# Optimization experiments

Measured on AMD Instinct MI355X. Metric: run time of the kernel, lower is better.

## Reference

```python
import jax, jax.numpy as jnp
import numpy as np
from jax import lax

# --- block geometry (matches init_kwargs) ---
B = 8
DIM = 192
HEADS = 6
KEY_DIM = DIM // HEADS  # 32, attn_ratio=1 so d == key_dim and dh == DIM
HX, WX = 32, 32         # search region
HZ, WZ = 16, 16         # template region
T = 1                   # template_number
L = HX * WX + T * HZ * WZ  # 1280 tokens
MLP_HIDDEN = int(DIM * 4.0)
BN_EPS = 1e-5


def _build_bias_idx():
    """Replicates Attention.__init__ global_att=True bias-index construction.
    Unique-offset ids may be permuted vs torch dict-insertion order, which is an
    equivalent reparameterization of the (randomly initialized) bias table."""
    g = np.stack(np.meshgrid(np.arange(HX), np.arange(WX), indexing='ij'), -1).reshape(-1, 2)
    pts = [g]
    for i in range(T):
        r = np.arange(HX + HZ * i, WX + WZ * (i + 1))
        g2 = np.stack(np.meshgrid(r, r, indexing='ij'), -1).reshape(-1, 2)
        pts.append(g2)
    p = np.concatenate(pts, 0)                      # (L, 2)
    off = np.abs(p[:, None, :] - p[None, :, :])     # (L, L, 2)
    key = off[:, :, 0].astype(np.int64) * 4096 + off[:, :, 1]
    uniq, inv = np.unique(key, return_inverse=True)
    return inv.reshape(L, L).astype(np.int32), int(len(uniq))


def setup_inputs() -> dict:
    key = jax.random.key(0)
    ks = jax.random.split(key, 16)
    idx_np, n_off = _build_bias_idx()
    s = 0.02
    return {
        'xz': jax.random.normal(ks[0], (B, L, DIM), jnp.float32),
        'bias_idx': jnp.asarray(idx_np),
        'ln1_g': jnp.ones((DIM,), jnp.float32),
        'ln1_b': jnp.zeros((DIM,), jnp.float32),
        'wqkv': jax.random.normal(ks[1], (DIM, 3 * DIM), jnp.float32) * s,
        'bqkv': jnp.zeros((3 * DIM,), jnp.float32),
        'wproj': jax.random.normal(ks[2], (DIM, DIM), jnp.float32) * s,
        'bproj': jnp.zeros((DIM,), jnp.float32),
        'bias_table': jax.random.normal(ks[3], (HEADS, n_off), jnp.float32) * 0.1,
        'conv_w': jax.random.normal(ks[4], (3, 3, 1, DIM), jnp.float32) * 0.1,  # depthwise HWIO
        'bn_scale': jnp.ones((DIM,), jnp.float32) + jax.random.normal(ks[5], (DIM,), jnp.float32) * 0.01,
        'bn_bias': jax.random.normal(ks[6], (DIM,), jnp.float32) * 0.01,
        'ln2_g': jnp.ones((DIM,), jnp.float32),
        'ln2_b': jnp.zeros((DIM,), jnp.float32),
        'w1': jax.random.normal(ks[7], (DIM, MLP_HIDDEN), jnp.float32) * s,
        'b1': jnp.zeros((MLP_HIDDEN,), jnp.float32),
        'w2': jax.random.normal(ks[8], (MLP_HIDDEN, DIM), jnp.float32) * s,
        'b2': jnp.zeros((DIM,), jnp.float32),
    }


def _layernorm(x, g, b, eps=1e-5):
    mu = jnp.mean(x, -1, keepdims=True)
    var = jnp.mean(jnp.square(x - mu), -1, keepdims=True)
    return (x - mu) * lax.rsqrt(var + eps) * g + b


def reference(xz, bias_idx, ln1_g, ln1_b, wqkv, bqkv, wproj, bproj, bias_table,
              conv_w, bn_scale, bn_bias, ln2_g, ln2_b, w1, b1, w2, b2):
    Bn, N, D = xz.shape
    scale = KEY_DIM ** -0.5
    # --- Attention (LeViT-style with gathered relative-position bias) ---
    h = _layernorm(xz, ln1_g, ln1_b)
    qkv = (h @ wqkv + bqkv).reshape(Bn, N, HEADS, 3 * KEY_DIM)
    q, k, v = jnp.split(qkv, 3, axis=3)            # each (B, N, H, key_dim)
    bias = bias_table[:, bias_idx]                  # (H, N, N) gather
    attn = jnp.einsum('bnhd,bmhd->bhnm', q, k) * scale + bias
    attn = jax.nn.softmax(attn, axis=-1)
    o = jnp.einsum('bhnm,bmhd->bnhd', attn, v).reshape(Bn, N, D)
    xm = xz + o @ wproj + bproj
    # --- depthwise local conv (Conv2d_BN, BN folded to scale/bias) per segment ---
    segs = []
    start = 0
    for (Hh, Ww) in [(HX, WX)] + [(HZ, WZ)] * T:
        xc = xm[:, start:start + Hh * Ww, :].reshape(Bn, Hh, Ww, D)
        xc = lax.conv_general_dilated(
            xc, conv_w, window_strides=(1, 1), padding='SAME',
            dimension_numbers=('NHWC', 'HWIO', 'NHWC'), feature_group_count=D)
        xc = xc * bn_scale + bn_bias
        segs.append(xc.reshape(Bn, Hh * Ww, D))
        start += Hh * Ww
    xm = jnp.concatenate(segs, axis=1)
    # --- MLP with pre-LN (exact GELU, matching nn.GELU default) ---
    m = _layernorm(xm, ln2_g, ln2_b)
    m = jax.nn.gelu(m @ w1 + b1, approximate=False) @ w2 + b2
    return xm + m
```

## Files before the change

### kernel.cpp

```cpp
#include <hip/hip_runtime.h>
#include <hip/hip_bf16.h>

#define BATCH 8
#define LTOK 1280
#define DIMC 192
#define HEADS 6
#define KD 32
#define HID 768
#define NROWS (BATCH*LTOK)

typedef short s16x8 __attribute__((ext_vector_type(8)));
typedef float f32x4 __attribute__((ext_vector_type(4)));
typedef unsigned short u16;

#define QS (0.17677669529663687f * 1.4426950408889634f)
#define L2E 1.4426950408889634f

__device__ __forceinline__ u16 f2bf(float x) {
    unsigned u = __float_as_uint(x);
    u = (u + 0x7FFFu + ((u >> 16) & 1u)) >> 16;
    return (u16)u;
}
__device__ __forceinline__ float bflo(unsigned u) { return __uint_as_float(u << 16); }
__device__ __forceinline__ float bfhi(unsigned u) { return __uint_as_float(u & 0xffff0000u); }
__device__ __forceinline__ float fexp2(float x) { float r; asm("v_exp_f32 %0, %1" : "=v"(r) : "v"(x)); return r; }
__device__ __forceinline__ float frcp(float x)  { float r; asm("v_rcp_f32 %0, %1" : "=v"(r) : "v"(x)); return r; }

__global__ __launch_bounds__(256) void pre_kernel(const float* w0, const float* w1,
                                                  const float* w2, const float* w3,
                                                  u16* o0, u16* o1, u16* o2, u16* o3,
                                                  const int* __restrict__ bidx,
                                                  const float* __restrict__ btab,
                                                  int n_off, u16* __restrict__ bm,
                                                  const float* __restrict__ xz,
                                                  const float* __restrict__ ln1g,
                                                  const float* __restrict__ ln1b,
                                                  u16* __restrict__ hbuf) {
    __shared__ float s[16][17];
    int f = blockIdx.x;
    if (f >= 3328) {
        int row = (f - 3328) * 4 + (threadIdx.x >> 6);
        int lane = threadIdx.x & 63;
        const float* xr = xz + (size_t)row * DIMC;
        float v0 = xr[lane], v1 = xr[lane + 64], v2 = xr[lane + 128];
        float sm = v0 + v1 + v2;
        float ss = v0 * v0 + v1 * v1 + v2 * v2;
        #pragma unroll
        for (int off = 32; off; off >>= 1) {
            sm += __shfl_xor(sm, off);
            ss += __shfl_xor(ss, off);
        }
        float mu  = sm * (1.0f / DIMC);
        float var = ss * (1.0f / DIMC) - mu * mu;
        float inv = rsqrtf(var + 1e-5f);
        u16* yr = hbuf + (size_t)row * DIMC;
        yr[lane]       = f2bf((v0 - mu) * inv * ln1g[lane]       + ln1b[lane]);
        yr[lane + 64]  = f2bf((v1 - mu) * inv * ln1g[lane + 64]  + ln1b[lane + 64]);
        yr[lane + 128] = f2bf((v2 - mu) * inv * ln1g[lane + 128] + ln1b[lane + 128]);
        return;
    }
    if (f >= 1728) {
        size_t flat = (size_t)(f - 1728) * 1024 + (size_t)threadIdx.x * 4;
        int4 iv = *(const int4*)(bidx + flat);
        #pragma unroll
        for (int h = 0; h < HEADS; ++h) {
            const float* tab = btab + (size_t)h * n_off;
            ushort4 o;
            o.x = f2bf(tab[iv.x] * L2E);
            o.y = f2bf(tab[iv.y] * L2E);
            o.z = f2bf(tab[iv.z] * L2E);
            o.w = f2bf(tab[iv.w] * L2E);
            *(ushort4*)(bm + (size_t)h * (LTOK * LTOK) + flat) = o;
        }
        return;
    }
    const float* in; u16* out; int K, N, tn, tk;
    if (f < 432)       { in = w0; out = o0; K = 192; N = 576; int r = f;        tn = r % 36; tk = r / 36; }
    else if (f < 576)  { in = w1; out = o1; K = 192; N = 192; int r = f - 432;  tn = r % 12; tk = r / 12; }
    else if (f < 1152) { in = w2; out = o2; K = 192; N = 768; int r = f - 576;  tn = r % 48; tk = r / 48; }
    else               { in = w3; out = o3; K = 768; N = 192; int r = f - 1152; tn = r % 12; tk = r / 12; }
    int tx = threadIdx.x & 15, ty = threadIdx.x >> 4;
    s[ty][tx] = in[(size_t)(tk * 16 + ty) * N + tn * 16 + tx];
    __syncthreads();
    out[(size_t)(tn * 16 + ty) * K + tk * 16 + tx] = f2bf(s[tx][ty]);
}

template<int ACT, int RES, int OBF, int QKV, int K, int MTILE>
__global__ __launch_bounds__(256) void gemm_mfma(const u16* __restrict__ A,
                                                 const u16* __restrict__ Wt,
                                                 const float* __restrict__ bias,
                                                 const float* __restrict__ R,
                                                 void* __restrict__ Cp,
                                                 u16* __restrict__ qb,
                                                 u16* __restrict__ kp,
                                                 u16* __restrict__ vp,
                                                 int N) {
    constexpr int SUB = MTILE / 64;
    int tid = threadIdx.x;
    int L = tid & 63, w = tid >> 6;
    int r = L & 15, g = L >> 4;
    int m0 = blockIdx.y * MTILE + w * (16 * SUB);
    int n0 = blockIdx.x * 64;

    f32x4 acc[SUB][4] = {};
    const u16* Ab = A + (size_t)(m0 + r) * K + g * 8;
    const u16* Wb = Wt + (size_t)(n0 + r) * K + g * 8;
    #pragma unroll 6
    for (int k0 = 0; k0 < K; k0 += 32) {
        s16x8 af[SUB];
        #pragma unroll
        for (int mi = 0; mi < SUB; ++mi)
            af[mi] = *(const s16x8*)(Ab + (size_t)mi * 16 * K + k0);
        #pragma unroll
        for (int nn = 0; nn < 4; ++nn) {
            s16x8 bf = *(const s16x8*)(Wb + (size_t)nn * 16 * K + k0);
            #pragma unroll
            for (int mi = 0; mi < SUB; ++mi)
                acc[mi][nn] = __builtin_amdgcn_mfma_f32_16x16x32_bf16(af[mi], bf, acc[mi][nn], 0, 0, 0);
        }
    }

    #pragma unroll
    for (int mi = 0; mi < SUB; ++mi)
    #pragma unroll
    for (int nn = 0; nn < 4; ++nn) {
        int cb = n0 + nn * 16;
        #pragma unroll
        for (int i = 0; i < 4; ++i) {
            int row = m0 + mi * 16 + g * 4 + i;
            float v = acc[mi][nn][i] + bias[cb + r];
            if (QKV) {
                int h  = cb / 96, c0 = cb % 96;
                int reg = c0 >> 5;
                if (reg == 0) {
                    v *= QS;
                    qb[(size_t)row * DIMC + h * 32 + (c0 & 31) + r] = f2bf(v);
                } else {
                    int b_ = row / LTOK, t = row - b_ * LTOK;
                    int T = t >> 5, it = t & 31;
                    int d = (c0 & 31) + r;
                    if (reg == 1) {
                        int which = (it >> 2) & 1;
                        int ik = ((it >> 3) << 2) | (it & 3);
                        int Lk = ((d >> 3) << 4) + ik;
                        kp[((size_t)(b_ * HEADS + h) * 40 + T) * 1024 + which * 512 + Lk * 8 + (d & 7)] = f2bf(v);
                    } else {
                        int Lv = ((it >> 3) << 4) + (d & 15);
                        vp[((size_t)(b_ * HEADS + h) * 40 + T) * 1024 + (d >> 4) * 512 + Lv * 8 + (it & 7)] = f2bf(v);
                    }
                }
            } else {
                if (ACT == 1) {
                    float u = v;
                    float y = 0.7978845608028654f * (u + 0.044715f * u * u * u);
                    float e2 = fexp2(y * 2.885390081777927f);
                    v = u - u * frcp(e2 + 1.0f);
                }
                if (RES) v += R[(size_t)row * N + cb + r];
                if (OBF) ((u16*)Cp)[(size_t)row * N + cb + r] = f2bf(v);
                else     ((float*)Cp)[(size_t)row * N + cb + r] = v;
            }
        }
    }
}

__global__ __launch_bounds__(256) void attn_mfma(const u16* __restrict__ qb,
                                                 const u16* __restrict__ kp,
                                                 const u16* __restrict__ vp,
                                                 const u16* __restrict__ bm,
                                                 u16* __restrict__ ob) {
    __shared__ __align__(16) u16 kvs[2][2][2048];
    int tid = threadIdx.x;
    int L = tid & 63, w = tid >> 6;
    int r = L & 15, g = L >> 4;
    int L8 = L * 8;

    int bid = blockIdx.x;
    int work = (bid & 7) * 120 + (bid >> 3);
    int b  = work & 7;
    int hq = work >> 3;
    int qt = (hq % 20) * 4 + w;
    int h  = hq / 20;

    s16x8 qf = *(const s16x8*)(qb + (size_t)(b * LTOK + qt * 16 + r) * DIMC + h * 32 + g * 8);

    int skv = w >> 1, half = w & 1;
    const u16* gs = (skv ? vp : kp) + (size_t)(b * HEADS + h) * 40 * 1024 + L8;
    u16* dst0 = &kvs[0][skv][half * 1024 + L8];
    u16* dst1 = &kvs[1][skv][half * 1024 + L8];

    const u16* bmr = bm + ((size_t)h * LTOK + qt * 16 + r) * LTOK + g * 8;

    f32x4 acc0 = {0.f, 0.f, 0.f, 0.f}, acc1 = {0.f, 0.f, 0.f, 0.f};
    float lsum = 0.f;

    {
        int4 pA = *(const int4*)(gs + half * 1024);
        int4 pB = *(const int4*)(gs + half * 1024 + 512);
        *(int4*)dst0 = pA;
        *(int4*)(dst0 + 512) = pB;
    }
    int4 bv0 = *(const int4*)(bmr);
    int4 bv1 = *(const int4*)(bmr + 32);
    __syncthreads();

    #pragma unroll 1
    for (int T = 0; T < 20; ++T) {
        int4 nA, nB, nb0, nb1;
        if (T < 19) {
            nA  = *(const int4*)(gs + (size_t)(2 * T + 2 + half) * 1024);
            nB  = *(const int4*)(gs + (size_t)(2 * T + 2 + half) * 1024 + 512);
            nb0 = *(const int4*)(bmr + (size_t)(T + 1) * 64);
            nb1 = *(const int4*)(bmr + (size_t)(T + 1) * 64 + 32);
        }
        const u16* kb = &kvs[T & 1][0][0];
        const u16* vb = &kvs[T & 1][1][0];
        f32x4 z0, z1, z2, z3;
        z0[0] = bflo(bv0.x); z0[1] = bfhi(bv0.x); z0[2] = bflo(bv0.y); z0[3] = bfhi(bv0.y);
        z1[0] = bflo(bv0.z); z1[1] = bfhi(bv0.z); z1[2] = bflo(bv0.w); z1[3] = bfhi(bv0.w);
        z2[0] = bflo(bv1.x); z2[1] = bfhi(bv1.x); z2[2] = bflo(bv1.y); z2[3] = bfhi(bv1.y);
        z3[0] = bflo(bv1.z); z3[1] = bfhi(bv1.z); z3[2] = bflo(bv1.w); z3[3] = bfhi(bv1.w);

        s16x8 kf0 = *(const s16x8*)(kb + L8);
        s16x8 kf1 = *(const s16x8*)(kb + 512 + L8);
        s16x8 kf2 = *(const s16x8*)(kb + 1024 + L8);
        s16x8 kf3 = *(const s16x8*)(kb + 1536 + L8);
        __builtin_amdgcn_s_setprio(1);
        f32x4 s0 = __builtin_amdgcn_mfma_f32_16x16x32_bf16(kf0, qf, z0, 0, 0, 0);
        f32x4 s1 = __builtin_amdgcn_mfma_f32_16x16x32_bf16(kf1, qf, z1, 0, 0, 0);
        f32x4 s2 = __builtin_amdgcn_mfma_f32_16x16x32_bf16(kf2, qf, z2, 0, 0, 0);
        f32x4 s3 = __builtin_amdgcn_mfma_f32_16x16x32_bf16(kf3, qf, z3, 0, 0, 0);
        float p[16];
        #pragma unroll
        for (int j = 0; j < 4; ++j) {
            p[j]      = fexp2(s0[j]);
            p[4 + j]  = fexp2(s1[j]);
            p[8 + j]  = fexp2(s2[j]);
            p[12 + j] = fexp2(s3[j]);
        }
        float t0 = ((p[0] + p[1]) + (p[2] + p[3])) + ((p[4] + p[5]) + (p[6] + p[7]));
        float t1 = ((p[8] + p[9]) + (p[10] + p[11])) + ((p[12] + p[13]) + (p[14] + p[15]));
        lsum += t0 + t1;
        union { unsigned u[4]; s16x8 v; } pa, pb;
        #pragma unroll
        for (int j = 0; j < 4; ++j) {
            asm("v_cvt_pk_bf16_f32 %0, %1, %2" : "=v"(pa.u[j]) : "v"(p[2 * j]), "v"(p[2 * j + 1]));
            asm("v_cvt_pk_bf16_f32 %0, %1, %2" : "=v"(pb.u[j]) : "v"(p[8 + 2 * j]), "v"(p[9 + 2 * j]));
        }
        s16x8 v0 = *(const s16x8*)(vb + L8);
        s16x8 v1 = *(const s16x8*)(vb + 512 + L8);
        s16x8 v2 = *(const s16x8*)(vb + 1024 + L8);
        s16x8 v3 = *(const s16x8*)(vb + 1536 + L8);
        acc0 = __builtin_amdgcn_mfma_f32_16x16x32_bf16(pa.v, v0, acc0, 0, 0, 0);
        acc1 = __builtin_amdgcn_mfma_f32_16x16x32_bf16(pa.v, v1, acc1, 0, 0, 0);
        acc0 = __builtin_amdgcn_mfma_f32_16x16x32_bf16(pb.v, v2, acc0, 0, 0, 0);
        acc1 = __builtin_amdgcn_mfma_f32_16x16x32_bf16(pb.v, v3, acc1, 0, 0, 0);
        __builtin_amdgcn_s_setprio(0);

        if (T < 19) {
            u16* d = (T & 1) ? dst0 : dst1;
            *(int4*)d = nA;
            *(int4*)(d + 512) = nB;
            bv0 = nb0; bv1 = nb1;
        }
        __syncthreads();
    }

    float lr = lsum;
    lr += __shfl_xor(lr, 16);
    lr += __shfl_xor(lr, 32);
    #pragma unroll
    for (int i = 0; i < 4; ++i) {
        float linv = frcp(__shfl(lr, 4 * g + i));
        size_t orow = (size_t)(b * LTOK + qt * 16 + 4 * g + i) * DIMC + h * 32 + r;
        ob[orow]      = f2bf(acc0[i] * linv);
        ob[orow + 16] = f2bf(acc1[i] * linv);
    }
}

__global__ __launch_bounds__(256) void conv_ln_kernel(const float* __restrict__ xm,
                                                      const float* __restrict__ w,
                                                      const float* __restrict__ scale,
                                                      const float* __restrict__ bias,
                                                      const float* __restrict__ g2,
                                                      const float* __restrict__ b2,
                                                      float* __restrict__ xm2,
                                                      u16* __restrict__ y) {
    int row = blockIdx.x * 4 + (threadIdx.x >> 6);
    int lane = threadIdx.x & 63;
    int b = row / LTOK, t = row - b * LTOK;
    int H, W, base, y0, x0;
    if (t < 1024) { H = 32; W = 32; base = 0;    y0 = t >> 5;            x0 = t & 31; }
    else          { H = 16; W = 16; base = 1024; int tt = t - 1024; y0 = tt >> 4; x0 = tt & 15; }
    float a0 = 0.f, a1 = 0.f, a2 = 0.f;
    #pragma unroll
    for (int ky = 0; ky < 3; ++ky) {
        int yy = y0 + ky - 1;
        if (yy < 0 || yy >= H) continue;
        #pragma unroll
        for (int kx = 0; kx < 3; ++kx) {
            int xx = x0 + kx - 1;
            if (xx < 0 || xx >= W) continue;
            const float* xr = xm + (size_t)(b * LTOK + base + yy * W + xx) * DIMC;
            const float* wr = w + (ky * 3 + kx) * DIMC;
            a0 += wr[lane]       * xr[lane];
            a1 += wr[lane + 64]  * xr[lane + 64];
            a2 += wr[lane + 128] * xr[lane + 128];
        }
    }
    float v0 = a0 * scale[lane]       + bias[lane];
    float v1 = a1 * scale[lane + 64]  + bias[lane + 64];
    float v2 = a2 * scale[lane + 128] + bias[lane + 128];
    float* xr2 = xm2 + (size_t)row * DIMC;
    xr2[lane] = v0; xr2[lane + 64] = v1; xr2[lane + 128] = v2;
    float s = v0 + v1 + v2;
    float ss = v0 * v0 + v1 * v1 + v2 * v2;
    #pragma unroll
    for (int off = 32; off; off >>= 1) {
        s  += __shfl_xor(s, off);
        ss += __shfl_xor(ss, off);
    }
    float mu  = s * (1.0f / DIMC);
    float var = ss * (1.0f / DIMC) - mu * mu;
    float inv = rsqrtf(var + 1e-5f);
    u16* yr = y + (size_t)row * DIMC;
    yr[lane]       = f2bf((v0 - mu) * inv * g2[lane]       + b2[lane]);
    yr[lane + 64]  = f2bf((v1 - mu) * inv * g2[lane + 64]  + b2[lane + 64]);
    yr[lane + 128] = f2bf((v2 - mu) * inv * g2[lane + 128] + b2[lane + 128]);
}

extern "C" void kernel_launch(void* const* d_in, const int* in_sizes, int n_in,
                              void* d_out, int out_size, void* d_ws, size_t ws_size,
                              hipStream_t stream) {
    const float* xz       = (const float*)d_in[0];
    const int*   bidx     = (const int*)  d_in[1];
    const float* ln1_g    = (const float*)d_in[2];
    const float* ln1_b    = (const float*)d_in[3];
    const float* wqkv     = (const float*)d_in[4];
    const float* bqkv     = (const float*)d_in[5];
    const float* wproj    = (const float*)d_in[6];
    const float* bproj    = (const float*)d_in[7];
    const float* btab     = (const float*)d_in[8];
    const float* conv_w   = (const float*)d_in[9];
    const float* bn_scale = (const float*)d_in[10];
    const float* bn_bias  = (const float*)d_in[11];
    const float* ln2_g    = (const float*)d_in[12];
    const float* ln2_b    = (const float*)d_in[13];
    const float* w1       = (const float*)d_in[14];
    const float* b1       = (const float*)d_in[15];
    const float* w2       = (const float*)d_in[16];
    const float* b2       = (const float*)d_in[17];
    int n_off = in_sizes[8] / HEADS;
    float* out = (float*)d_out;

    char* wsb = (char*)d_ws;
    u16*  hbuf   = (u16*)(wsb + 0);
    u16*  ob     = (u16*)(wsb + 0);
    u16*  wqkvT  = (u16*)(wsb + 3932160);
    u16*  wprojT = (u16*)(wsb + 4153344);
    u16*  w1T    = (u16*)(wsb + 4227072);
    u16*  w2T    = (u16*)(wsb + 4521984);
    u16*  bm     = (u16*)(wsb + 4816896);
    u16*  hid    = (u16*)(wsb + 4816896);
    u16*  kp     = (u16*)(wsb + 24477696);
    u16*  vp     = (u16*)(wsb + 28409856);
    float* xm2   = (float*)(wsb + 24477696);
    u16*  qb     = (u16*)(wsb + 32342016);
    float* xm    = (float*)(wsb + 32342016);

    pre_kernel<<<1728 + LTOK * LTOK / 1024 + NROWS / 4, 256, 0, stream>>>(
        wqkv, wproj, w1, w2, wqkvT, wprojT, w1T, w2T, bidx, btab, n_off, bm,
        xz, ln1_g, ln1_b, hbuf);
    gemm_mfma<0,0,0,1,DIMC,256><<<dim3(576 / 64, NROWS / 256), 256, 0, stream>>>(
        hbuf, wqkvT, bqkv, nullptr, nullptr, qb, kp, vp, 3 * DIMC);
    attn_mfma<<<960, 256, 0, stream>>>(qb, kp, vp, bm, ob);
    gemm_mfma<0,1,0,0,DIMC,128><<<dim3(DIMC / 64, NROWS / 128), 256, 0, stream>>>(
        ob, wprojT, bproj, xz, xm, nullptr, nullptr, nullptr, DIMC);
    conv_ln_kernel<<<NROWS / 4, 256, 0, stream>>>(
        xm, conv_w, bn_scale, bn_bias, ln2_g, ln2_b, xm2, hbuf);
    gemm_mfma<1,0,1,0,DIMC,256><<<dim3(HID / 64, NROWS / 256), 256, 0, stream>>>(
        hbuf, w1T, b1, nullptr, hid, nullptr, nullptr, nullptr, HID);
    gemm_mfma<0,1,0,0,HID,128><<<dim3(DIMC / 64, NROWS / 128), 256, 0, stream>>>(
        hid, w2T, b2, xm2, out, nullptr, nullptr, nullptr, DIMC);
}
```

Baseline: 128.9 us.

## Pre-pack bias in MFMA fragment order and software-pipeline QK score MFMAs

The relative-position bias matrix is now gathered into a per-(head, query-tile) packed layout that matches the MFMA accumulator fragment order, so each lane in the attention kernel reads contiguous 16-byte chunks instead of strided rows. The pre-kernel launches more blocks, each handling one head per block, in place of looping over all heads. In the attention loop, the QK^T MFMAs for the next tile are issued right after the barrier, overlapping them with the softmax and PV work of the loop structure. This trades more gather blocks and index recomputation in the pre-kernel for better bias-load coalescing and cross-iteration overlap.

```diff
diff --git a/kernel.cpp b/kernel.cpp
--- a/kernel.cpp
+++ b/kernel.cpp
@@ -31,15 +31,15 @@
                                                   u16* o0, u16* o1, u16* o2, u16* o3,
                                                   const int* __restrict__ bidx,
                                                   const float* __restrict__ btab,
-                                                  int n_off, u16* __restrict__ bm,
+                                                  int n_off, u16* __restrict__ bmp,
                                                   const float* __restrict__ xz,
                                                   const float* __restrict__ ln1g,
                                                   const float* __restrict__ ln1b,
                                                   u16* __restrict__ hbuf) {
     __shared__ float s[16][17];
     int f = blockIdx.x;
-    if (f >= 3328) {
-        int row = (f - 3328) * 4 + (threadIdx.x >> 6);
+    if (f >= 11328) {
+        int row = (f - 11328) * 4 + (threadIdx.x >> 6);
         int lane = threadIdx.x & 63;
         const float* xr = xz + (size_t)row * DIMC;
         float v0 = xr[lane], v1 = xr[lane + 64], v2 = xr[lane + 128];
@@ -60,18 +60,22 @@
         return;
     }
     if (f >= 1728) {
-        size_t flat = (size_t)(f - 1728) * 1024 + (size_t)threadIdx.x * 4;
-        int4 iv = *(const int4*)(bidx + flat);
-        #pragma unroll
-        for (int h = 0; h < HEADS; ++h) {
-            const float* tab = btab + (size_t)h * n_off;
-            ushort4 o;
-            o.x = f2bf(tab[iv.x] * L2E);
-            o.y = f2bf(tab[iv.y] * L2E);
-            o.z = f2bf(tab[iv.z] * L2E);
-            o.w = f2bf(tab[iv.w] * L2E);
-            *(ushort4*)(bm + (size_t)h * (LTOK * LTOK) + flat) = o;
-        }
+        int fb = f - 1728;
+        int qt = fb / 120;
+        int rem = fb - qt * 120;
+        int T = rem / 6, h = rem - (rem / 6) * 6;
+        int tid = threadIdx.x;
+        int half = tid >> 7, L = (tid >> 1) & 63, j4 = (tid & 1) * 4;
+        int n = qt * 16 + (L & 15);
+        int m = T * 64 + half * 32 + ((L >> 4) << 3) + j4;
+        int4 iv = *(const int4*)(bidx + (size_t)n * LTOK + m);
+        const float* tab = btab + (size_t)h * n_off;
+        ushort4 o;
+        o.x = f2bf(tab[iv.x] * L2E);
+        o.y = f2bf(tab[iv.y] * L2E);
+        o.z = f2bf(tab[iv.z] * L2E);
+        o.w = f2bf(tab[iv.w] * L2E);
+        *(ushort4*)(bmp + (size_t)(h * 80 + qt) * 20480 + T * 1024 + tid * 4) = o;
         return;
     }
     const float* in; u16* out; int K, N, tn, tk;
@@ -167,7 +171,7 @@
 __global__ __launch_bounds__(256) void attn_mfma(const u16* __restrict__ qb,
                                                  const u16* __restrict__ kp,
                                                  const u16* __restrict__ vp,
-                                                 const u16* __restrict__ bm,
+                                                 const u16* __restrict__ bmp,
                                                  u16* __restrict__ ob) {
     __shared__ __align__(16) u16 kvs[2][2][2048];
     int tid = threadIdx.x;
@@ -189,7 +193,7 @@
     u16* dst0 = &kvs[0][skv][half * 1024 + L8];
     u16* dst1 = &kvs[1][skv][half * 1024 + L8];
 
-    const u16* bmr = bm + ((size_t)h * LTOK + qt * 16 + r) * LTOK + g * 8;
+    const u16* bmr = bmp + (size_t)(h * 80 + qt) * 20480 + L8;
 
     f32x4 acc0 = {0.f, 0.f, 0.f, 0.f}, acc1 = {0.f, 0.f, 0.f, 0.f};
     float lsum = 0.f;
@@ -200,9 +204,27 @@
         *(int4*)dst0 = pA;
         *(int4*)(dst0 + 512) = pB;
     }
-    int4 bv0 = *(const int4*)(bmr);
-    int4 bv1 = *(const int4*)(bmr + 32);
+    int4 cb0 = *(const int4*)(bmr);
+    int4 cb1 = *(const int4*)(bmr + 512);
     __syncthreads();
+
+    f32x4 s0, s1, s2, s3;
+    {
+        const u16* kb = &kvs[0][0][0];
+        f32x4 z0, z1, z2, z3;
+        z0[0] = bflo(cb0.x); z0[1] = bfhi(cb0.x); z0[2] = bflo(cb0.y); z0[3] = bfhi(cb0.y);
+        z1[0] = bflo(cb0.z); z1[1] = bfhi(cb0.z); z1[2] = bflo(cb0.w); z1[3] = bfhi(cb0.w);
+        z2[0] = bflo(cb1.x); z2[1] = bfhi(cb1.x); z2[2] = bflo(cb1.y); z2[3] = bfhi(cb1.y);
+        z3[0] = bflo(cb1.z); z3[1] = bfhi(cb1.z); z3[2] = bflo(cb1.w); z3[3] = bfhi(cb1.w);
+        s16x8 kf0 = *(const s16x8*)(kb + L8);
+        s16x8 kf1 = *(const s16x8*)(kb + 512 + L8);
+        s16x8 kf2 = *(const s16x8*)(kb + 1024 + L8);
+        s16x8 kf3 = *(const s16x8*)(kb + 1536 + L8);
+        s0 = __builtin_amdgcn_mfma_f32_16x16x32_bf16(kf0, qf, z0, 0, 0, 0);
+        s1 = __builtin_amdgcn_mfma_f32_16x16x32_bf16(kf1, qf, z1, 0, 0, 0);
+        s2 = __builtin_amdgcn_mfma_f32_16x16x32_bf16(kf2, qf, z2, 0, 0, 0);
+        s3 = __builtin_amdgcn_mfma_f32_16x16x32_bf16(kf3, qf, z3, 0, 0, 0);
+    }
 
     #pragma unroll 1
     for (int T = 0; T < 20; ++T) {
@@ -210,26 +232,10 @@
         if (T < 19) {
             nA  = *(const int4*)(gs + (size_t)(2 * T + 2 + half) * 1024);
             nB  = *(const int4*)(gs + (size_t)(2 * T + 2 + half) * 1024 + 512);
-            nb0 = *(const int4*)(bmr + (size_t)(T + 1) * 64);
-            nb1 = *(const int4*)(bmr + (size_t)(T + 1) * 64 + 32);
-        }
-        const u16* kb = &kvs[T & 1][0][0];
-        const u16* vb = &kvs[T & 1][1][0];
-        f32x4 z0, z1, z2, z3;
-        z0[0] = bflo(bv0.x); z0[1] = bfhi(bv0.x); z0[2] = bflo(bv0.y); z0[3] = bfhi(bv0.y);
-        z1[0] = bflo(bv0.z); z1[1] = bfhi(bv0.z); z1[2] = bflo(bv0.w); z1[3] = bfhi(bv0.w);
-        z2[0] = bflo(bv1.x); z2[1] = bfhi(bv1.x); z2[2] = bflo(bv1.y); z2[3] = bfhi(bv1.y);
-        z3[0] = bflo(bv1.z); z3[1] = bfhi(bv1.z); z3[2] = bflo(bv1.w); z3[3] = bfhi(bv1.w);
-
-        s16x8 kf0 = *(const s16x8*)(kb + L8);
-        s16x8 kf1 = *(const s16x8*)(kb + 512 + L8);
-        s16x8 kf2 = *(const s16x8*)(kb + 1024 + L8);
-        s16x8 kf3 = *(const s16x8*)(kb + 1536 + L8);
+            nb0 = *(const int4*)(bmr + (size_t)(T + 1) * 1024);
+            nb1 = *(const int4*)(bmr + (size_t)(T + 1) * 1024 + 512);
+        }
         __builtin_amdgcn_s_setprio(1);
-        f32x4 s0 = __builtin_amdgcn_mfma_f32_16x16x32_bf16(kf0, qf, z0, 0, 0, 0);
-        f32x4 s1 = __builtin_amdgcn_mfma_f32_16x16x32_bf16(kf1, qf, z1, 0, 0, 0);
-        f32x4 s2 = __builtin_amdgcn_mfma_f32_16x16x32_bf16(kf2, qf, z2, 0, 0, 0);
-        f32x4 s3 = __builtin_amdgcn_mfma_f32_16x16x32_bf16(kf3, qf, z3, 0, 0, 0);
         float p[16];
         #pragma unroll
         for (int j = 0; j < 4; ++j) {
@@ -247,6 +253,7 @@
             asm("v_cvt_pk_bf16_f32 %0, %1, %2" : "=v"(pa.u[j]) : "v"(p[2 * j]), "v"(p[2 * j + 1]));
             asm("v_cvt_pk_bf16_f32 %0, %1, %2" : "=v"(pb.u[j]) : "v"(p[8 + 2 * j]), "v"(p[9 + 2 * j]));
         }
+        const u16* vb = &kvs[T & 1][1][0];
         s16x8 v0 = *(const s16x8*)(vb + L8);
         s16x8 v1 = *(const s16x8*)(vb + 512 + L8);
         s16x8 v2 = *(const s16x8*)(vb + 1024 + L8);
@@ -261,9 +268,26 @@
             u16* d = (T & 1) ? dst0 : dst1;
             *(int4*)d = nA;
             *(int4*)(d + 512) = nB;
-            bv0 = nb0; bv1 = nb1;
         }
         __syncthreads();
+        if (T < 19) {
+            const u16* kb = &kvs[(T + 1) & 1][0][0];
+            f32x4 z0, z1, z2, z3;
+            z0[0] = bflo(nb0.x); z0[1] = bfhi(nb0.x); z0[2] = bflo(nb0.y); z0[3] = bfhi(nb0.y);
+            z1[0] = bflo(nb0.z); z1[1] = bfhi(nb0.z); z1[2] = bflo(nb0.w); z1[3] = bfhi(nb0.w);
+            z2[0] = bflo(nb1.x); z2[1] = bfhi(nb1.x); z2[2] = bflo(nb1.y); z2[3] = bfhi(nb1.y);
+            z3[0] = bflo(nb1.z); z3[1] = bfhi(nb1.z); z3[2] = bflo(nb1.w); z3[3] = bfhi(nb1.w);
+            s16x8 kf0 = *(const s16x8*)(kb + L8);
+            s16x8 kf1 = *(const s16x8*)(kb + 512 + L8);
+            s16x8 kf2 = *(const s16x8*)(kb + 1024 + L8);
+            s16x8 kf3 = *(const s16x8*)(kb + 1536 + L8);
+            __builtin_amdgcn_s_setprio(1);
+            s0 = __builtin_amdgcn_mfma_f32_16x16x32_bf16(kf0, qf, z0, 0, 0, 0);
+            s1 = __builtin_amdgcn_mfma_f32_16x16x32_bf16(kf1, qf, z1, 0, 0, 0);
+            s2 = __builtin_amdgcn_mfma_f32_16x16x32_bf16(kf2, qf, z2, 0, 0, 0);
+            s3 = __builtin_amdgcn_mfma_f32_16x16x32_bf16(kf3, qf, z3, 0, 0, 0);
+            __builtin_amdgcn_s_setprio(0);
+        }
     }
 
     float lr = lsum;
@@ -360,7 +384,7 @@
     u16*  wprojT = (u16*)(wsb + 4153344);
     u16*  w1T    = (u16*)(wsb + 4227072);
     u16*  w2T    = (u16*)(wsb + 4521984);
-    u16*  bm     = (u16*)(wsb + 4816896);
+    u16*  bmp    = (u16*)(wsb + 4816896);
     u16*  hid    = (u16*)(wsb + 4816896);
     u16*  kp     = (u16*)(wsb + 24477696);
     u16*  vp     = (u16*)(wsb + 28409856);
@@ -368,12 +392,12 @@
     u16*  qb     = (u16*)(wsb + 32342016);
     float* xm    = (float*)(wsb + 32342016);
 
-    pre_kernel<<<1728 + LTOK * LTOK / 1024 + NROWS / 4, 256, 0, stream>>>(
-        wqkv, wproj, w1, w2, wqkvT, wprojT, w1T, w2T, bidx, btab, n_off, bm,
+    pre_kernel<<<13888, 256, 0, stream>>>(
+        wqkv, wproj, w1, w2, wqkvT, wprojT, w1T, w2T, bidx, btab, n_off, bmp,
         xz, ln1_g, ln1_b, hbuf);
     gemm_mfma<0,0,0,1,DIMC,256><<<dim3(576 / 64, NROWS / 256), 256, 0, stream>>>(
         hbuf, wqkvT, bqkv, nullptr, nullptr, qb, kp, vp, 3 * DIMC);
-    attn_mfma<<<960, 256, 0, stream>>>(qb, kp, vp, bm, ob);
+    attn_mfma<<<960, 256, 0, stream>>>(qb, kp, vp, bmp, ob);
     gemm_mfma<0,1,0,0,DIMC,128><<<dim3(DIMC / 64, NROWS / 128), 256, 0, stream>>>(
         ob, wprojT, bproj, xz, xm, nullptr, nullptr, nullptr, DIMC);
     conv_ln_kernel<<<NROWS / 4, 256, 0, stream>>>(
```

New measurement: 124.2 us. 3.6% less time.
